# Kernel tuning notes

Measured on AMD Instinct MI355X. Metric: run time of the kernel, lower is better.

The kernel has to match this reference:

```python
import jax, jax.numpy as jnp
import numpy as np

NUM_HEADS = 16
EPS = 1e-6


def _ln(t, w, b):
    # LayerNorm over last dim (head_dim), elementwise affine, eps=1e-6
    mu = jnp.mean(t, axis=-1, keepdims=True)
    var = jnp.mean(jnp.square(t - mu), axis=-1, keepdims=True)
    return (t - mu) * jax.lax.rsqrt(var + EPS) * w + b


def setup_inputs() -> dict:
    key = jax.random.key(0)
    ks = jax.random.split(key, 10)
    b, s1, s2, qdim, kdim = 2, 2048, 3072, 1024, 1024
    d = qdim // NUM_HEADS
    x = jax.random.normal(ks[0], (b, s1, qdim), dtype=jnp.float32)
    y = jax.random.normal(ks[1], (b, s2, kdim), dtype=jnp.float32)
    padding_mask = jax.random.randint(ks[2], (b, s2), 0, 2) > 0
    # guarantee at least one valid key per row (avoid all -inf softmax rows)
    padding_mask = padding_mask.at[:, 0].set(True)
    w = 0.02
    Wq = jax.random.normal(ks[3], (qdim, qdim), dtype=jnp.float32) * w
    bq = jnp.zeros((qdim,), jnp.float32)
    Wkv = jax.random.normal(ks[4], (2 * qdim, kdim), dtype=jnp.float32) * w
    bkv = jnp.zeros((2 * qdim,), jnp.float32)
    qn_w = jnp.ones((d,), jnp.float32)
    qn_b = jnp.zeros((d,), jnp.float32)
    kn_w = jnp.ones((d,), jnp.float32)
    kn_b = jnp.zeros((d,), jnp.float32)
    Wo = jax.random.normal(ks[5], (qdim, qdim), dtype=jnp.float32) * w
    bo = jnp.zeros((qdim,), jnp.float32)
    return {"x": x, "y": y, "padding_mask": padding_mask,
            "Wq": Wq, "bq": bq, "Wkv": Wkv, "bkv": bkv,
            "qn_w": qn_w, "qn_b": qn_b, "kn_w": kn_w, "kn_b": kn_b,
            "Wo": Wo, "bo": bo}


def reference(x, y, padding_mask, Wq, bq, Wkv, bkv, qn_w, qn_b, kn_w, kn_b, Wo, bo):
    b, s1, c = x.shape
    s2 = y.shape[1]
    h, d = NUM_HEADS, c // NUM_HEADS
    scale = d ** (-0.5)
    q = (x @ Wq.T + bq).reshape(b, s1, h, d)
    kv = (y @ Wkv.T + bkv).reshape(b, s2, 2, h, d)
    k, v = kv[:, :, 0], kv[:, :, 1]  # (b, s2, h, d)
    q = _ln(q, qn_w, qn_b) * scale
    k = _ln(k, kn_w, kn_b)
    attn = jnp.einsum('bihd,bjhd->bhij', q, k)  # (b, h, s1, s2)
    attn = jnp.where(padding_mask[:, None, None, :], attn, -jnp.inf)
    p = jax.nn.softmax(attn, axis=-1)
    ctx = jnp.einsum('bhij,bjhd->bihd', p, v).reshape(b, s1, c)
    out = ctx @ Wo.T + bo
    return out
```

## Files before the change

### kernel.cpp

```cpp
#include <hip/hip_runtime.h>
#include <stdint.h>
#include <stddef.h>

typedef __attribute__((ext_vector_type(4))) float  f32x4;
typedef __attribute__((ext_vector_type(8))) short  short8;
typedef __attribute__((ext_vector_type(4))) short  short4v;
typedef __attribute__((ext_vector_type(2))) unsigned int uint2v;

__device__ __forceinline__ unsigned short f2bfbits(float f) {
  unsigned int u = __builtin_bit_cast(unsigned int, f);
  u += 0x7FFFu + ((u >> 16) & 1u);
  return (unsigned short)(u >> 16);
}

__device__ __forceinline__ f32x4 mfma16(short8 a, short8 b, f32x4 c) {
  return __builtin_amdgcn_mfma_f32_16x16x32_bf16(a, b, c, 0, 0, 0);
}

__device__ __forceinline__ unsigned int cvtpk(float a, float b) {
  unsigned int r;
  asm volatile("v_cvt_pk_bf16_f32 %0, %1, %2" : "=v"(r) : "v"(a), "v"(b));
  return r;
}

__device__ __forceinline__ void gload16(const void* g, void* l) {
  __builtin_amdgcn_global_load_lds(
      (const __attribute__((address_space(1))) void*)g,
      (__attribute__((address_space(3))) void*)l, 16, 0, 0);
}

__device__ __forceinline__ void cvt_block(const float* __restrict__ in,
                                          unsigned short* __restrict__ out,
                                          int blk, int t) {
  size_t i = (size_t)blk * 256 + t;
  f32x4 a = *(const f32x4*)(in + i * 8);
  f32x4 b = *(const f32x4*)(in + i * 8 + 4);
  short8 o;
  o[0] = (short)f2bfbits(a[0]); o[1] = (short)f2bfbits(a[1]);
  o[2] = (short)f2bfbits(a[2]); o[3] = (short)f2bfbits(a[3]);
  o[4] = (short)f2bfbits(b[0]); o[5] = (short)f2bfbits(b[1]);
  o[6] = (short)f2bfbits(b[2]); o[7] = (short)f2bfbits(b[3]);
  *(short8*)(out + i * 8) = o;
}

__global__ __launch_bounds__(256) void fused_prep(
    const float* __restrict__ x, unsigned short* __restrict__ xb,
    const float* __restrict__ y, unsigned short* __restrict__ yb,
    const float* __restrict__ Wq, unsigned short* __restrict__ Wqb,
    const float* __restrict__ Wkv, unsigned short* __restrict__ Wkvb,
    const float* __restrict__ Wo, unsigned short* __restrict__ Wob,
    const unsigned char* __restrict__ mraw, float* __restrict__ maddC,
    int* __restrict__ perm, int* __restrict__ invperm,
    int* __restrict__ nvalid) {
  const int bid = blockIdx.x, t = threadIdx.x;
  if (bid < 2048)       { cvt_block(x,   xb,   bid,        t); return; }
  else if (bid < 5120)  { cvt_block(y,   yb,   bid - 2048, t); return; }
  else if (bid < 5632)  { cvt_block(Wq,  Wqb,  bid - 5120, t); return; }
  else if (bid < 6656)  { cvt_block(Wkv, Wkvb, bid - 5632, t); return; }
  else if (bid < 7168)  { cvt_block(Wo,  Wob,  bid - 6656, t); return; }

  const int batch = bid - 7168;
  __shared__ int s_na, s_gt, s_m84;
  if (t == 0) { s_na = 0; s_gt = 0; s_m84 = 0; }
  __syncthreads();
  int na = 0, gt = 0, m84 = 0;
  for (int i = t; i < 4096; i += 256) {
    unsigned char v = mraw[i];
    if (v) {
      if (i & 3) na++;
      if ((i & 7) == 4) m84++;
      if (v > 1) gt++;
    }
  }
  atomicAdd(&s_na, na); atomicAdd(&s_gt, gt); atomicAdd(&s_m84, m84);
  __syncthreads();
  int layout;
  if (s_na == 0) layout = s_m84 ? 1 : 3;
  else           layout = s_gt ? 2 : 0;

  const int base = batch * 3072;
  int myv[12];
  int cnt = 0;
#pragma unroll
  for (int k = 0; k < 12; k++) {
    int j = t * 12 + k;
    int gj = base + j;
    bool mv;
    if (layout == 0)      mv = mraw[gj] != 0;
    else if (layout == 1) mv = ((const int*)mraw)[gj] != 0;
    else if (layout == 2) mv = ((const float*)mraw)[gj] > 0.5f;
    else                  mv = ((const long long*)mraw)[gj] != 0;
    myv[k] = mv ? 1 : 0;
    cnt += myv[k];
  }
  const int lane = t & 63, wv = t >> 6;
  int inc = cnt;
#pragma unroll
  for (int d = 1; d < 64; d <<= 1) {
    int n = __shfl_up(inc, d);
    if (lane >= d) inc += n;
  }
  __shared__ int wsum[4];
  if (lane == 63) wsum[wv] = inc;
  __syncthreads();
  int woff = 0;
#pragma unroll
  for (int i2 = 0; i2 < 4; i2++) if (i2 < wv) woff += wsum[i2];
  const int total = wsum[0] + wsum[1] + wsum[2] + wsum[3];
  int vp = woff + inc - cnt;
  if (t == 0) nvalid[batch] = total;
#pragma unroll
  for (int k = 0; k < 12; k++) {
    int j = t * 12 + k;
    int slot = myv[k] ? vp : (total + (j - vp));
    perm[base + j] = slot;
    invperm[base + slot] = j;
    vp += myv[k];
  }
  for (int jj = t; jj < 3072; jj += 256)
    maddC[base + jj] = (jj < total) ? -10.0f : -1e30f;
}

__global__ __launch_bounds__(256) void gemm_qkv(
    const unsigned short* __restrict__ xb, const unsigned short* __restrict__ Wqb,
    const float* __restrict__ bq, const float* __restrict__ qnw,
    const float* __restrict__ qnb, unsigned short* __restrict__ qln,
    const unsigned short* __restrict__ yb, const unsigned short* __restrict__ Wkvb,
    const float* __restrict__ bkv, const float* __restrict__ knw,
    const float* __restrict__ knb, unsigned short* __restrict__ kln,
    unsigned short* __restrict__ vrow, const int* __restrict__ perm) {
  __shared__ unsigned short As[128 * 64];
  __shared__ unsigned short Bs[128 * 64];
  const int t = threadIdx.x, l = t & 63, w = t >> 6;
  const int lo = l & 15, hi = l >> 4;
  const int wr = w >> 1, wc = w & 1;
  const int bid = blockIdx.x;
  const int isq = bid < 256;
  const int bn = isq ? (bid & 7) : ((bid - 256) & 15);
  const int bm = isq ? (bid >> 3) : ((bid - 256) >> 4);
  const unsigned short* A = isq ? xb : yb;
  const unsigned short* B = isq ? Wqb : Wkvb;
  const float* bias = isq ? bq : bkv;
  const float* lnw = isq ? qnw : knw;
  const float* lnb = isq ? qnb : knb;
  unsigned short* bfout = isq ? qln : kln;
  const float lnscale = isq ? 0.125f * 1.44269504f : 1.0f;
  const int rpb = isq ? 2048 : 3072;
  const int K = 1024;

  const int sr = l >> 3;
  const int sc = ((l & 7) ^ sr) << 3;
  const unsigned short* Ab = A + (size_t)bm * 128 * K + (size_t)sr * K + sc;
  const unsigned short* Bb = B + (size_t)bn * 128 * K + (size_t)sr * K + sc;

  f32x4 acc[4][4] = {};

  for (int kt = 0; kt < K; kt += 64) {
    __syncthreads();
#pragma unroll
    for (int p = 0; p < 4; ++p) {
      int c = w * 4 + p;
      gload16(Ab + (size_t)c * 8 * K + kt, &As[c * 512]);
      gload16(Bb + (size_t)c * 8 * K + kt, &Bs[c * 512]);
    }
    __syncthreads();
#pragma unroll
    for (int kk = 0; kk < 2; ++kk) {
      short8 af[4], bf[4];
#pragma unroll
      for (int i = 0; i < 4; ++i) {
        int slot = (((kk * 4 + hi) ^ (lo & 7)) << 3);
        af[i] = *(const short8*)&As[(wr * 64 + i * 16 + lo) * 64 + slot];
        bf[i] = *(const short8*)&Bs[(wc * 64 + i * 16 + lo) * 64 + slot];
      }
#pragma unroll
      for (int i = 0; i < 4; ++i)
#pragma unroll
        for (int j = 0; j < 4; ++j)
          acc[i][j] = mfma16(af[i], bf[j], acc[i][j]);
    }
  }

  float bv[4];
#pragma unroll
  for (int j = 0; j < 4; ++j) bv[j] = bias[bn * 128 + wc * 64 + j * 16 + lo];
#pragma unroll
  for (int i = 0; i < 4; ++i)
#pragma unroll
    for (int j = 0; j < 4; ++j)
#pragma unroll
      for (int r = 0; r < 4; ++r) acc[i][j][r] += bv[j];

  if (!isq && bn >= 8) {
#pragma unroll
    for (int j = 0; j < 4; ++j) {
      int col = bn * 128 + wc * 64 + j * 16 + lo;
      int vcol = col - 1024;
#pragma unroll
      for (int i = 0; i < 4; ++i) {
        int row = bm * 128 + wr * 64 + i * 16 + hi * 4;
#pragma unroll
        for (int r = 0; r < 4; ++r)
          vrow[(size_t)(row + r) * 1024 + vcol] = f2bfbits(acc[i][j][r]);
      }
    }
  } else {
    float gwv[4], gbv[4];
#pragma unroll
    for (int j = 0; j < 4; ++j) {
      gwv[j] = lnw[j * 16 + lo];
      gbv[j] = lnb[j * 16 + lo];
    }
    const int hcol = (bn * 128 + wc * 64) >> 6;
#pragma unroll
    for (int i = 0; i < 4; ++i) {
#pragma unroll
      for (int r = 0; r < 4; ++r) {
        float s1 = (acc[i][0][r] + acc[i][1][r]) + (acc[i][2][r] + acc[i][3][r]);
        float s2 = (acc[i][0][r] * acc[i][0][r] + acc[i][1][r] * acc[i][1][r]) +
                   (acc[i][2][r] * acc[i][2][r] + acc[i][3][r] * acc[i][3][r]);
#pragma unroll
        for (int m = 1; m < 16; m <<= 1) {
          s1 += __shfl_xor(s1, m);
          s2 += __shfl_xor(s2, m);
        }
        float mu = s1 * 0.015625f;
        float var = fmaxf(s2 * 0.015625f - mu * mu, 0.0f);
        float rq = rsqrtf(var + 1e-6f);
        int row = bm * 128 + wr * 64 + i * 16 + hi * 4 + r;
        int bb = row >= rpb;
        int rr = row - bb * rpb;
        int rrs = isq ? rr : perm[bb * 3072 + rr];
        size_t base = ((size_t)(bb * 16 + hcol) * rpb + rrs) * 64;
#pragma unroll
        for (int j = 0; j < 4; ++j)
          bfout[base + j * 16 + lo] =
              f2bfbits(((acc[i][j][r] - mu) * rq * gwv[j] + gbv[j]) * lnscale);
      }
    }
  }
}

__global__ __launch_bounds__(256) void v_tr(
    const unsigned short* __restrict__ vrow, const int* __restrict__ invperm,
    unsigned short* __restrict__ vt) {
  __shared__ unsigned short tile[64][65];
  const int jt = blockIdx.x, h = blockIdx.y;
  const int b = jt / 48, j0 = (jt % 48) * 64;
  const int t = threadIdx.x;
  const int r = t >> 2, c0 = (t & 3) << 4;
  const int sj = invperm[b * 3072 + j0 + r];
  const unsigned short* src = vrow + ((size_t)b * 3072 + sj) * 1024 + h * 64 + c0;
  *(short8*)&tile[r][c0]     = *(const short8*)src;
  *(short8*)&tile[r][c0 + 8] = *(const short8*)(src + 8);
  __syncthreads();
  const int d = t >> 2, jc = (t & 3) << 4;
  unsigned short* dst = vt + ((size_t)((b * 16 + h) * 64 + d)) * 3072 + j0 + jc;
  short8 o0, o1;
#pragma unroll
  for (int i = 0; i < 8; i++) o0[i] = tile[jc + i][d];
#pragma unroll
  for (int i = 0; i < 8; i++) o1[i] = tile[jc + 8 + i][d];
  *(short8*)dst = o0;
  *(short8*)(dst + 8) = o1;
}

__global__ __launch_bounds__(512) void gemm_out(
    const unsigned short* __restrict__ A, const unsigned short* __restrict__ B,
    const float* __restrict__ bias, float* __restrict__ C, int N, int K) {
  __shared__ unsigned short As[128 * 64];
  __shared__ unsigned short Bs[128 * 64];
  const int t = threadIdx.x, l = t & 63, w = t >> 6;
  const int lo = l & 15, hi = l >> 4;
  const int wr = w >> 1, wc = w & 1;
  const int bn = blockIdx.x, bm = blockIdx.y;

  const int sr = l >> 3;
  const int sc = ((l & 7) ^ sr) << 3;
  const unsigned short* Ab = A + (size_t)bm * 128 * K + (size_t)sr * K + sc;
  const unsigned short* Bb = B + (size_t)bn * 128 * K + (size_t)sr * K + sc;

  f32x4 acc[2][4] = {};

  for (int kt = 0; kt < K; kt += 64) {
    __syncthreads();
#pragma unroll
    for (int p = 0; p < 2; ++p) {
      int c = p * 8 + w;
      gload16(Ab + (size_t)c * 8 * K + kt, &As[c * 512]);
      gload16(Bb + (size_t)c * 8 * K + kt, &Bs[c * 512]);
    }
    __syncthreads();
#pragma unroll
    for (int kk = 0; kk < 2; ++kk) {
      short8 af[2], bf[4];
#pragma unroll
      for (int i = 0; i < 2; ++i) {
        int slot = (((kk * 4 + hi) ^ (lo & 7)) << 3);
        af[i] = *(const short8*)&As[(wr * 32 + i * 16 + lo) * 64 + slot];
      }
#pragma unroll
      for (int j = 0; j < 4; ++j) {
        int slot = (((kk * 4 + hi) ^ (lo & 7)) << 3);
        bf[j] = *(const short8*)&Bs[(wc * 64 + j * 16 + lo) * 64 + slot];
      }
#pragma unroll
      for (int i = 0; i < 2; ++i)
#pragma unroll
        for (int j = 0; j < 4; ++j)
          acc[i][j] = mfma16(af[i], bf[j], acc[i][j]);
    }
  }

#pragma unroll
  for (int j = 0; j < 4; ++j) {
    int col = bn * 128 + wc * 64 + j * 16 + lo;
    float bv = bias[col];
#pragma unroll
    for (int i = 0; i < 2; ++i) {
      int row = bm * 128 + wr * 32 + i * 16 + hi * 4;
#pragma unroll
      for (int r = 0; r < 4; ++r)
        C[(size_t)(row + r) * N + col] = acc[i][j][r] + bv;
    }
  }
}

__global__ __launch_bounds__(256, 4) void attn_fwd(
    const unsigned short* __restrict__ Q, const unsigned short* __restrict__ Kn,
    const unsigned short* __restrict__ Vt, const float* __restrict__ maskAdd,
    const int* __restrict__ nva, unsigned short* __restrict__ ctx) {
  int flat = blockIdx.y * 32 + blockIdx.x;
  int f = (flat & 7) * 128 + (flat >> 3);
  const int bh = f >> 5, qb = f & 31;
  const int b = bh >> 4, h = bh & 15;
  const int t = threadIdx.x, l = t & 63, w = t >> 6;
  const int lo = l & 15, hi = l >> 4;
  const int q0 = qb * 64 + w * 16;

  const int nv = nva[b];
  const int kend = (nv + 63) & ~63;

  __shared__ unsigned short lds[20480];
  unsigned short* Ks = lds;
  unsigned short* Vs = lds + 8192;
  unsigned short* P  = lds + 16384 + w * 1024;

  const unsigned short* Qh = Q + ((size_t)bh * 2048 + q0) * 64;
  const unsigned short* Kb = Kn + (size_t)bh * 3072 * 64;
  const unsigned short* Vb = Vt + (size_t)bh * 64 * 3072;
  const float* mb = maskAdd + b * 3072;

  const int srow = w * 8 + (l >> 3);
  const int swz8 = ((l & 7) ^ ((l >> 3) & 7)) << 3;
  const unsigned short* kS = Kb + (size_t)srow * 64 + swz8;
  const unsigned short* vS = Vb + (size_t)srow * 3072 + swz8;
  const int dstoff = w * 512;

  short8 qf[2];
#pragma unroll
  for (int g = 0; g < 2; g++)
    qf[g] = *(const short8*)(Qh + (size_t)lo * 64 + g * 32 + hi * 8);

  f32x4 O[4] = {};
  f32x4 lacc = {};
  const int myswz = (lo & 7) << 3;

  short8 paR[2] = {};
  short8 vfR[4][2] = {};

#pragma unroll
  for (int j = 0; j < 2; ++j) {
    gload16(kS + (size_t)j * 2048, Ks + j * 2048 + dstoff);
    gload16(vS + (size_t)j * 98304, Vs + j * 2048 + dstoff);
  }
  __syncthreads();

  for (int kt = 0; kt < kend; kt += 64) {
    const int cur = (kt >> 6) & 1;
    const int nxt = cur ^ 1;
    const int ktn = (kt + 64 < kend) ? kt + 64 : 0;
#pragma unroll
    for (int j = 0; j < 2; ++j) {
      gload16(kS + (size_t)ktn * 64 + (size_t)j * 2048,
              Ks + nxt * 4096 + j * 2048 + dstoff);
      gload16(vS + ktn + (size_t)j * 98304,
              Vs + nxt * 4096 + j * 2048 + dstoff);
    }

    const unsigned short* Kc = Ks + cur * 4096;
    const unsigned short* Vc = Vs + cur * 4096;

    f32x4 s[4];
#pragma unroll
    for (int nf = 0; nf < 4; nf++)
      s[nf] = *(const f32x4*)(mb + kt + nf * 16 + hi * 4);
    __builtin_amdgcn_s_setprio(1);
#pragma unroll
    for (int nf = 0; nf < 4; nf++) {
      const int row = nf * 16 + lo;
      short8 k0 = *(const short8*)&Kc[row * 64 + ((hi * 8) ^ myswz)];
      short8 k1 = *(const short8*)&Kc[row * 64 + ((32 + hi * 8) ^ myswz)];
      s[nf] = mfma16(k0, qf[0], s[nf]);
      s[nf] = mfma16(k1, qf[1], s[nf]);
    }

#pragma unroll
    for (int df = 0; df < 4; df++)
#pragma unroll
      for (int ks = 0; ks < 2; ks++)
        O[df] = mfma16(paR[ks], vfR[df][ks], O[df]);
    __builtin_amdgcn_s_setprio(0);

#pragma unroll
    for (int nf = 0; nf < 4; nf++)
#pragma unroll
      for (int r = 0; r < 4; r++)
        s[nf][r] = __builtin_amdgcn_exp2f(s[nf][r]);
    lacc += (s[0] + s[1]) + (s[2] + s[3]);

#pragma unroll
    for (int nf = 0; nf < 4; nf++) {
      uint2v u;
      u.x = cvtpk(s[nf][0], s[nf][1]);
      u.y = cvtpk(s[nf][2], s[nf][3]);
      *(uint2v*)&P[lo * 64 + ((nf * 16 + hi * 4) ^ myswz)] = u;
    }
#pragma unroll
    for (int ks = 0; ks < 2; ks++)
      paR[ks] = *(const short8*)&P[lo * 64 + ((ks * 32 + hi * 8) ^ myswz)];
#pragma unroll
    for (int df = 0; df < 4; df++) {
      const int row = df * 16 + lo;
#pragma unroll
      for (int ks = 0; ks < 2; ks++)
        vfR[df][ks] = *(const short8*)&Vc[row * 64 + ((ks * 32 + hi * 8) ^ myswz)];
    }

    __syncthreads();
  }

  __builtin_amdgcn_s_setprio(1);
#pragma unroll
  for (int df = 0; df < 4; df++)
#pragma unroll
    for (int ks = 0; ks < 2; ks++)
      O[df] = mfma16(paR[ks], vfR[df][ks], O[df]);
  __builtin_amdgcn_s_setprio(0);

  float lr = (lacc[0] + lacc[1]) + (lacc[2] + lacc[3]);
  lr += __shfl_xor(lr, 16);
  lr += __shfl_xor(lr, 32);

  float i0 = 1.0f / __shfl(lr, hi * 4 + 0);
  float i1 = 1.0f / __shfl(lr, hi * 4 + 1);
  float i2 = 1.0f / __shfl(lr, hi * 4 + 2);
  float i3 = 1.0f / __shfl(lr, hi * 4 + 3);
  size_t rbase = (size_t)b * 2048 + q0 + hi * 4;
#pragma unroll
  for (int df = 0; df < 4; df++) {
    int cc = h * 64 + df * 16 + lo;
    ctx[(rbase + 0) * 1024 + cc] = f2bfbits(O[df][0] * i0);
    ctx[(rbase + 1) * 1024 + cc] = f2bfbits(O[df][1] * i1);
    ctx[(rbase + 2) * 1024 + cc] = f2bfbits(O[df][2] * i2);
    ctx[(rbase + 3) * 1024 + cc] = f2bfbits(O[df][3] * i3);
  }
}

extern "C" void kernel_launch(void* const* d_in, const int* in_sizes, int n_in,
                              void* d_out, int out_size, void* d_ws, size_t ws_size,
                              hipStream_t stream) {
  const float* x   = (const float*)d_in[0];
  const float* y   = (const float*)d_in[1];
  const unsigned char* pmask = (const unsigned char*)d_in[2];
  const float* Wq  = (const float*)d_in[3];
  const float* bq  = (const float*)d_in[4];
  const float* Wkv = (const float*)d_in[5];
  const float* bkv = (const float*)d_in[6];
  const float* qnw = (const float*)d_in[7];
  const float* qnb = (const float*)d_in[8];
  const float* knw = (const float*)d_in[9];
  const float* knb = (const float*)d_in[10];
  const float* Wo  = (const float*)d_in[11];
  const float* bo  = (const float*)d_in[12];
  float* out = (float*)d_out;

  const size_t MB = 1024ull * 1024ull;
  char* ws = (char*)d_ws;
  float* maddC         = (float*)ws;
  int*   perm          = (int*)(ws + 24576);
  int*   invperm       = (int*)(ws + 49152);
  int*   nvalid        = (int*)(ws + 73728);
  char*  wb            = ws + 131072;
  unsigned short* Wqb  = (unsigned short*)(wb);
  unsigned short* Wkvb = (unsigned short*)(wb + 2 * MB);
  unsigned short* Wob  = (unsigned short*)(wb + 6 * MB);
  unsigned short* qln  = (unsigned short*)(wb + 8 * MB);
  unsigned short* kln  = (unsigned short*)(wb + 16 * MB);
  unsigned short* vt   = (unsigned short*)(wb + 28 * MB);
  unsigned short* ctxb = (unsigned short*)(wb + 40 * MB);
  unsigned short* yb   = (unsigned short*)(wb + 48 * MB);
  unsigned short* xb   = (unsigned short*)(wb + 60 * MB);
  unsigned short* vrow = (unsigned short*)(wb + 68 * MB);
  if (ws_size < 131072 + 80 * MB) return;

  fused_prep<<<dim3(7170), dim3(256), 0, stream>>>(
      x, xb, y, yb, Wq, Wqb, Wkv, Wkvb, Wo, Wob, pmask, maddC, perm, invperm,
      nvalid);

  gemm_qkv<<<dim3(1024), dim3(256), 0, stream>>>(
      xb, Wqb, bq, qnw, qnb, qln, yb, Wkvb, bkv, knw, knb, kln, vrow, perm);

  v_tr<<<dim3(96, 16), dim3(256), 0, stream>>>(vrow, invperm, vt);

  attn_fwd<<<dim3(32, 32), dim3(256), 0, stream>>>(qln, kln, vt, maddC, nvalid, ctxb);

  gemm_out<<<dim3(8, 32), dim3(512), 0, stream>>>(ctxb, Wob, bo, out, 1024, 1024);
}
```

Before: 151.5 us.

## Gather K rows via invperm in attention instead of scattering in QKV GEMM

The QKV GEMM now writes normalized K rows in natural order rather than scattering them through a perm table, and the perm array is dropped. The attention kernel instead gathers K rows through invperm on each tile load, prefetching the index one tile ahead. The QKV GEMM block index is also remapped so neighbouring blocks share weight tiles, which should improve L2 reuse. The gather adds index loads and non-contiguous row reads inside the attention loop, in exchange for contiguous stores in the GEMM epilogue.

```diff
diff --git a/kernel.cpp b/kernel.cpp
--- a/kernel.cpp
+++ b/kernel.cpp
@@ -50,8 +50,7 @@
     const float* __restrict__ Wkv, unsigned short* __restrict__ Wkvb,
     const float* __restrict__ Wo, unsigned short* __restrict__ Wob,
     const unsigned char* __restrict__ mraw, float* __restrict__ maddC,
-    int* __restrict__ perm, int* __restrict__ invperm,
-    int* __restrict__ nvalid) {
+    int* __restrict__ invperm, int* __restrict__ nvalid) {
   const int bid = blockIdx.x, t = threadIdx.x;
   if (bid < 2048)       { cvt_block(x,   xb,   bid,        t); return; }
   else if (bid < 5120)  { cvt_block(y,   yb,   bid - 2048, t); return; }
@@ -113,7 +112,6 @@
   for (int k = 0; k < 12; k++) {
     int j = t * 12 + k;
     int slot = myv[k] ? vp : (total + (j - vp));
-    perm[base + j] = slot;
     invperm[base + slot] = j;
     vp += myv[k];
   }
@@ -128,16 +126,19 @@
     const unsigned short* __restrict__ yb, const unsigned short* __restrict__ Wkvb,
     const float* __restrict__ bkv, const float* __restrict__ knw,
     const float* __restrict__ knb, unsigned short* __restrict__ kln,
-    unsigned short* __restrict__ vrow, const int* __restrict__ perm) {
+    unsigned short* __restrict__ vrow) {
   __shared__ unsigned short As[128 * 64];
   __shared__ unsigned short Bs[128 * 64];
   const int t = threadIdx.x, l = t & 63, w = t >> 6;
   const int lo = l & 15, hi = l >> 4;
   const int wr = w >> 1, wc = w & 1;
-  const int bid = blockIdx.x;
-  const int isq = bid < 256;
-  const int bn = isq ? (bid & 7) : ((bid - 256) & 15);
-  const int bm = isq ? (bid >> 3) : ((bid - 256) >> 4);
+  const int flat = blockIdx.x;
+  int vb;
+  if (flat < 256) vb = (flat & 7) * 32 + (flat >> 3);
+  else { int f2 = flat - 256; vb = 256 + (f2 & 7) * 96 + (f2 >> 3); }
+  const int isq = vb < 256;
+  const int bn = isq ? (vb & 7) : ((vb - 256) & 15);
+  const int bm = isq ? (vb >> 3) : ((vb - 256) >> 4);
   const unsigned short* A = isq ? xb : yb;
   const unsigned short* B = isq ? Wqb : Wkvb;
   const float* bias = isq ? bq : bkv;
@@ -230,8 +231,7 @@
         int row = bm * 128 + wr * 64 + i * 16 + hi * 4 + r;
         int bb = row >= rpb;
         int rr = row - bb * rpb;
-        int rrs = isq ? rr : perm[bb * 3072 + rr];
-        size_t base = ((size_t)(bb * 16 + hcol) * rpb + rrs) * 64;
+        size_t base = ((size_t)(bb * 16 + hcol) * rpb + rr) * 64;
 #pragma unroll
         for (int j = 0; j < 4; ++j)
           bfout[base + j * 16 + lo] =
@@ -327,9 +327,10 @@
 }
 
 __global__ __launch_bounds__(256, 4) void attn_fwd(
-    const unsigned short* __restrict__ Q, const unsigned short* __restrict__ Kn,
+    const unsigned short* __restrict__ Q, const unsigned short* __restrict__ KnU,
     const unsigned short* __restrict__ Vt, const float* __restrict__ maskAdd,
-    const int* __restrict__ nva, unsigned short* __restrict__ ctx) {
+    const int* __restrict__ invperm, const int* __restrict__ nva,
+    unsigned short* __restrict__ ctx) {
   int flat = blockIdx.y * 32 + blockIdx.x;
   int f = (flat & 7) * 128 + (flat >> 3);
   const int bh = f >> 5, qb = f & 31;
@@ -347,13 +348,13 @@
   unsigned short* P  = lds + 16384 + w * 1024;
 
   const unsigned short* Qh = Q + ((size_t)bh * 2048 + q0) * 64;
-  const unsigned short* Kb = Kn + (size_t)bh * 3072 * 64;
+  const unsigned short* KbU = KnU + (size_t)bh * 3072 * 64;
   const unsigned short* Vb = Vt + (size_t)bh * 64 * 3072;
   const float* mb = maskAdd + b * 3072;
+  const int ibase = b * 3072;
 
   const int srow = w * 8 + (l >> 3);
   const int swz8 = ((l & 7) ^ ((l >> 3) & 7)) << 3;
-  const unsigned short* kS = Kb + (size_t)srow * 64 + swz8;
   const unsigned short* vS = Vb + (size_t)srow * 3072 + swz8;
   const int dstoff = w * 512;
 
@@ -369,10 +370,16 @@
   short8 paR[2] = {};
   short8 vfR[4][2] = {};
 
-#pragma unroll
-  for (int j = 0; j < 2; ++j) {
-    gload16(kS + (size_t)j * 2048, Ks + j * 2048 + dstoff);
-    gload16(vS + (size_t)j * 98304, Vs + j * 2048 + dstoff);
+  int rs0 = invperm[ibase + srow];
+  int rs1 = invperm[ibase + 32 + srow];
+  gload16(KbU + (size_t)rs0 * 64 + swz8, Ks + dstoff);
+  gload16(KbU + (size_t)rs1 * 64 + swz8, Ks + 2048 + dstoff);
+  gload16(vS, Vs + dstoff);
+  gload16(vS + 98304, Vs + 2048 + dstoff);
+  {
+    int kt1 = (64 < kend) ? 64 : 0;
+    rs0 = invperm[ibase + kt1 + srow];
+    rs1 = invperm[ibase + kt1 + 32 + srow];
   }
   __syncthreads();
 
@@ -380,12 +387,14 @@
     const int cur = (kt >> 6) & 1;
     const int nxt = cur ^ 1;
     const int ktn = (kt + 64 < kend) ? kt + 64 : 0;
-#pragma unroll
-    for (int j = 0; j < 2; ++j) {
-      gload16(kS + (size_t)ktn * 64 + (size_t)j * 2048,
-              Ks + nxt * 4096 + j * 2048 + dstoff);
-      gload16(vS + ktn + (size_t)j * 98304,
-              Vs + nxt * 4096 + j * 2048 + dstoff);
+    gload16(KbU + (size_t)rs0 * 64 + swz8, Ks + nxt * 4096 + dstoff);
+    gload16(KbU + (size_t)rs1 * 64 + swz8, Ks + nxt * 4096 + 2048 + dstoff);
+    gload16(vS + ktn, Vs + nxt * 4096 + dstoff);
+    gload16(vS + ktn + 98304, Vs + nxt * 4096 + 2048 + dstoff);
+    {
+      int ktn2 = (kt + 128 < kend) ? kt + 128 : 0;
+      rs0 = invperm[ibase + ktn2 + srow];
+      rs1 = invperm[ibase + ktn2 + 32 + srow];
     }
 
     const unsigned short* Kc = Ks + cur * 4096;
@@ -488,9 +497,8 @@
   const size_t MB = 1024ull * 1024ull;
   char* ws = (char*)d_ws;
   float* maddC         = (float*)ws;
-  int*   perm          = (int*)(ws + 24576);
-  int*   invperm       = (int*)(ws + 49152);
-  int*   nvalid        = (int*)(ws + 73728);
+  int*   invperm       = (int*)(ws + 24576);
+  int*   nvalid        = (int*)(ws + 49152);
   char*  wb            = ws + 131072;
   unsigned short* Wqb  = (unsigned short*)(wb);
   unsigned short* Wkvb = (unsigned short*)(wb + 2 * MB);
@@ -505,15 +513,16 @@
   if (ws_size < 131072 + 80 * MB) return;
 
   fused_prep<<<dim3(7170), dim3(256), 0, stream>>>(
-      x, xb, y, yb, Wq, Wqb, Wkv, Wkvb, Wo, Wob, pmask, maddC, perm, invperm,
+      x, xb, y, yb, Wq, Wqb, Wkv, Wkvb, Wo, Wob, pmask, maddC, invperm,
       nvalid);
 
   gemm_qkv<<<dim3(1024), dim3(256), 0, stream>>>(
-      xb, Wqb, bq, qnw, qnb, qln, yb, Wkvb, bkv, knw, knb, kln, vrow, perm);
+      xb, Wqb, bq, qnw, qnb, qln, yb, Wkvb, bkv, knw, knb, kln, vrow);
 
   v_tr<<<dim3(96, 16), dim3(256), 0, stream>>>(vrow, invperm, vt);
 
-  attn_fwd<<<dim3(32, 32), dim3(256), 0, stream>>>(qln, kln, vt, maddC, nvalid, ctxb);
+  attn_fwd<<<dim3(32, 32), dim3(256), 0, stream>>>(qln, kln, vt, maddC,
+                                                   invperm, nvalid, ctxb);
 
   gemm_out<<<dim3(8, 32), dim3(512), 0, stream>>>(ctxb, Wob, bo, out, 1024, 1024);
 }
```

New measurement: 147.0 us. 2.9% less time.
